# Performance work log

Measured on AMD Instinct MI355X. Metric: run time of the kernel, lower is better.

## Reference

```python
import jax, jax.numpy as jnp
import numpy as np

# ---- module config (init_kwargs) ----
B, CIN, H, W_ = 2, 64, 56, 56
COUT, KH, KW = 128, 3, 3
K = CIN * KH * KW               # 576, reduction dim
ARRAY_ROWS = 128
IN_SLICES = (2, 2, 2, 2)        # 8-bit inputs, 2-bit slices
W_SLICES = (2, 2, 2, 2)         # 8-bit weights, 2-bit slices
N_STEPS_IN = 2 ** sum(IN_SLICES)    # 256, unsigned quantizer
N_STEPS_W = 2 ** sum(W_SLICES)      # 256
ADC_BINS = 256
ADC_STEP = 4.0

def _shifts_masks(slices):
    masks, shifts = [], [0]
    for s in slices[::-1]:
        masks.append((1 << s) - 1)
        shifts.append(s + shifts[-1])
    return np.array(shifts[-2::-1], np.int32), np.array(masks[::-1], np.int32)

_ish, _im = _shifts_masks(IN_SLICES)
_wsh, _wm = _shifts_masks(W_SLICES)
ISH, IM = jnp.asarray(_ish), jnp.asarray(_im)
WSH, WM = jnp.asarray(_wsh), jnp.asarray(_wm)
ISF = jnp.asarray((1 << _ish).astype(np.float32))  # slice recombine weights 2^shift
WSF = jnp.asarray((1 << _wsh).astype(np.float32))


def setup_inputs() -> dict:
    key = jax.random.key(0)
    k1, k2 = jax.random.split(key)
    return {
        "x": jax.random.normal(k1, (B, CIN, H, W_), jnp.float32),
        "w": jax.random.normal(k2, (COUT, CIN, KH, KW), jnp.float32),
    }


def _im2col(x):
    # 3x3 SAME conv patches, ordering [Cin, kh, kw] to match w.reshape(COUT, K)
    xp = jnp.pad(x, ((0, 0), (0, 0), (1, 1), (1, 1)))
    cols = jnp.stack([xp[:, :, i:i + H, j:j + W_]
                      for i in range(KH) for j in range(KW)], axis=2)  # [B,Cin,9,H,W]
    return cols.transpose(0, 3, 4, 1, 2).reshape(B * H * W_, K)  # [Nx, K]


def _quant_unsigned(v, n_steps):
    # Quantizer.offset + Quantizer.forward (unsigned, per-row over dim=-1)
    offs = v.min(axis=-1, keepdims=True)
    vr = v - offs
    step = vr.max(axis=-1, keepdims=True) / (n_steps - 1)
    q = jnp.round(jnp.clip(vr, 0.0, step * n_steps) / step).astype(jnp.int32)
    return q, step[..., 0], offs[..., 0]


def _slice_bits(q, shifts, masks):
    # Slicer.forward: stack (q >> shift) & mask along new leading slice dim
    s = shifts.reshape((-1,) + (1,) * q.ndim)
    m = masks.reshape((-1,) + (1,) * q.ndim)
    return (q[None] >> s) & m


def _chunk(t):
    # Chunker.forward over last dim K
    nb = -(-K // ARRAY_ROWS)
    npb = -(-K // nb)
    pad = nb * npb - K
    t = jnp.pad(t, [(0, 0)] * (t.ndim - 1) + [(0, pad)])
    t = t.reshape(t.shape[:-1] + (nb, npb))
    return jnp.moveaxis(t, -2, 0)  # [nb, ..., npb]


def reference(x, w):
    xf = _im2col(x)                    # [Nx, K]
    wf = w.reshape(COUT, K)            # [Ny, K]
    x_sum = xf.sum(axis=-1)            # [Nx]
    w_sum = wf.sum(axis=-1)            # [Ny]

    xq, x_scale, x_offs = _quant_unsigned(xf, N_STEPS_IN)
    wq, w_scale, w_offs = _quant_unsigned(wf, N_STEPS_W)

    xc = _chunk(_slice_bits(xq, ISH, IM))  # [nb, nis, Nx, npb] int32
    wc = _chunk(_slice_bits(wq, WSH, WM))  # [nb, nws, Ny, npb] int32

    # bit-serial crossbar MACs per (chunk, weight-slice, input-slice)
    z = jnp.einsum('bixk,bwyk->bwixy',
                   xc.astype(jnp.float32), wc.astype(jnp.float32))  # [nb,nws,nis,Nx,Ny]

    # ADC digitization (unsigned, fixed step): quantize then dequantize
    z = jnp.round(jnp.clip(z, 0.0, ADC_STEP * ADC_BINS) / ADC_STEP) * ADC_STEP

    # Chunker.reverse: sum crossbar blocks; Slicer.reverse: shift-weighted sums
    z = z.sum(axis=0)                               # [nws,nis,Nx,Ny]
    z = jnp.einsum('wixy,w,i->xy', z, WSF, ISF)     # [Nx,Ny]

    # dequantize scales and unsigned-offset correction:
    # x.y = sx*sy*(xq.yq) + x_offs*sum(y) + y_offs*sum(x) - x_offs*y_offs*K
    z = z * x_scale[:, None] * w_scale[None, :]
    z = (z + x_offs[:, None] * w_sum[None, :]
           + w_offs[None, :] * x_sum[:, None]
           - x_offs[:, None] * w_offs[None, :] * K)

    return z.reshape(B, H, W_, COUT).transpose(0, 3, 1, 2)  # [B,Cout,H,W]
```

## Files before the change

### kernel.cpp

```cpp
#include <hip/hip_runtime.h>


#define NXROW 6272
#define KDIM  576
#define NPB   116
#define SSTR  656

typedef int i32x4 __attribute__((ext_vector_type(4)));

__device__ __forceinline__ i32x4 slice2b(i32x4 v, int sh) {
    i32x4 r;
    r[0] = (int)(((unsigned)v[0] >> sh) & 0x03030303u);
    r[1] = (int)(((unsigned)v[1] >> sh) & 0x03030303u);
    r[2] = (int)(((unsigned)v[2] >> sh) & 0x03030303u);
    r[3] = (int)(((unsigned)v[3] >> sh) & 0x03030303u);
    return r;
}

__global__ __launch_bounds__(256) void k_q(
    const float* __restrict__ x, const float* __restrict__ w,
    unsigned char* __restrict__ Xq, unsigned char* __restrict__ Wq,
    float* __restrict__ xsc, float* __restrict__ xof, float* __restrict__ xsm,
    float* __restrict__ wsc, float* __restrict__ wof, float* __restrict__ wsm)
{
    __shared__ __align__(16) unsigned char scr[4][SSTR];

    int tid = threadIdx.x, wv = tid >> 6, lane = tid & 63;
    int W = blockIdx.x * 4 + wv;
    unsigned char* myrow = scr[wv];

    if (lane < 16) {
        int col = lane < 12 ? (lane / 3) * 128 + 116 + (lane % 3) * 4
                            : 624 + (lane - 12) * 4;
        *(unsigned int*)(myrow + col) = 0u;
    }

    float v[9];
    unsigned char* dstbase;
    int rl;
    float *sc, *of, *sm;
    int sidx;

    if (W < NXROW) {
        int b = W >= 3136 ? 1 : 0;
        int pos = W - b * 3136;
        int hg = pos / 56, wg = pos - hg * 56;
        const float* xb = x + (size_t)(b * 64) * 3136;
#pragma unroll
        for (int r = 0; r < 9; r++) {
            int k = r * 64 + lane;
            int cin = k / 9;
            int off = k - cin * 9;
            int kh = off / 3;
            int kw = off - kh * 3;
            int hr = hg - 1 + kh, wc = wg - 1 + kw;
            bool ok = ((unsigned)hr < 56u) && ((unsigned)wc < 56u);
            v[r] = ok ? xb[cin * 3136 + hr * 56 + wc] : 0.f;
        }
        dstbase = Xq + (size_t)(W >> 4) * 10240;  rl = W & 15;
        sc = xsc; of = xof; sm = xsm; sidx = W;
    } else {
        int row = W - NXROW;
        const float* wr = w + (size_t)row * KDIM;
#pragma unroll
        for (int r = 0; r < 9; r++) v[r] = wr[r * 64 + lane];
        dstbase = Wq + (size_t)(row >> 4) * 10240;  rl = row & 15;
        sc = wsc; of = wof; sm = wsm; sidx = row;
    }

    float mn = v[0], mx = v[0], s = 0.f;
#pragma unroll
    for (int r = 0; r < 9; r++) { mn = fminf(mn, v[r]); mx = fmaxf(mx, v[r]); s += v[r]; }
#pragma unroll
    for (int off2 = 1; off2 < 64; off2 <<= 1) {
        mn = fminf(mn, __shfl_xor(mn, off2));
        mx = fmaxf(mx, __shfl_xor(mx, off2));
        s += __shfl_xor(s, off2);
    }
    float step = (mx - mn) / 255.0f;
    if (lane == 0) { sc[sidx] = step; of[sidx] = mn; sm[sidx] = s; }

#pragma unroll
    for (int r = 0; r < 9; r++) {
        int q = (int)rintf((v[r] - mn) / step);
        q = q < 0 ? 0 : (q > 255 ? 255 : q);
        int k = r * 64 + lane;
        int ch = k / NPB;
        myrow[k + 12 * ch] = (unsigned char)q;
    }
    __syncthreads();

    if (lane < 40) {
        int u = lane;
        i32x4 seg = *(const i32x4*)(myrow + u * 16);
        int dst16 = (u >> 3) * 128 + ((u >> 2) & 1) * 64 + (u & 3) * 16 + rl;
        *(i32x4*)(dstbase + (size_t)dst16 * 16) = seg;
    }
}

__global__ __launch_bounds__(256) void k_d(
    const unsigned char* __restrict__ Xq, const unsigned char* __restrict__ Wq,
    const float* __restrict__ xscg, const float* __restrict__ xofg,
    const float* __restrict__ xsmg,
    const float* __restrict__ wscg, const float* __restrict__ wofg,
    const float* __restrict__ wsmg, float* __restrict__ out)
{
    __shared__ __align__(16) int pacc[4][64][4];

    int tid = threadIdx.x, wv = tid >> 6, lane = tid & 63;
    int g = lane >> 4, i16 = lane & 15;
    int blk = blockIdx.x;
    int ct = blk & 7, rtile = blk >> 3;
    const unsigned char* xt = Xq + (size_t)rtile * 10240 + lane * 16;
    const unsigned char* wt = Wq + (size_t)ct * 10240 + lane * 16;

    int ish = 6 - 2 * wv;
    const i32x4 zero = {0, 0, 0, 0};
    i32x4 acc4[4] = {{0,0,0,0},{0,0,0,0},{0,0,0,0},{0,0,0,0}};

#pragma unroll
    for (int ch = 0; ch < 5; ch++) {
        i32x4 x0 = *(const i32x4*)(xt + ch * 2048);
        i32x4 x1 = *(const i32x4*)(xt + ch * 2048 + 1024);
        i32x4 w0 = *(const i32x4*)(wt + ch * 2048);
        i32x4 w1 = *(const i32x4*)(wt + ch * 2048 + 1024);
        i32x4 a0 = slice2b(x0, ish), a1 = slice2b(x1, ish);
#pragma unroll
        for (int ws = 0; ws < 4; ws++) {
            i32x4 b0 = slice2b(w0, 6 - 2 * ws);
            i32x4 b1 = slice2b(w1, 6 - 2 * ws);
            i32x4 d = __builtin_amdgcn_mfma_i32_16x16x64_i8(b0, a0, zero, 0, 0, 0);
            d = __builtin_amdgcn_mfma_i32_16x16x64_i8(b1, a1, d, 0, 0, 0);
            int sh = ish + 6 - 2 * ws;
#pragma unroll
            for (int r = 0; r < 4; r++) {
                int z = d[r];
                z = z > 1024 ? 1024 : z;
                int t = (z >> 2) & 1;
                int r4 = (z + 1 + t) & ~3;
                acc4[ws][r] += r4 << sh;
            }
        }
    }

    i32x4 acc;
#pragma unroll
    for (int r = 0; r < 4; r++)
        acc[r] = (acc4[0][r] + acc4[1][r]) + (acc4[2][r] + acc4[3][r]);

    if (wv != 0) *(i32x4*)&pacc[wv][lane][0] = acc;
    __syncthreads();

    if (wv == 0) {
        i32x4 p1 = *(const i32x4*)&pacc[1][lane][0];
        i32x4 p2 = *(const i32x4*)&pacc[2][lane][0];
        i32x4 p3 = *(const i32x4*)&pacc[3][lane][0];
#pragma unroll
        for (int r = 0; r < 4; r++)
            acc[r] = (acc[r] + p1[r]) + (p2[r] + p3[r]);

        int b = rtile >= 196 ? 1 : 0;
        int xrow = rtile * 16 + i16;
        float xs_ = xscg[xrow], xo = xofg[xrow], xsv = xsmg[xrow];
        int hw = (rtile - 196 * b) * 16 + i16;
#pragma unroll
        for (int r = 0; r < 4; r++) {
            int wrow = ct * 16 + g * 4 + r;
            float tt = ((float)acc[r] * xs_) * wscg[wrow];
            float res = ((tt + xo * wsmg[wrow]) + wofg[wrow] * xsv)
                      - (xo * wofg[wrow]) * 576.0f;
            out[(size_t)(b * 128 + wrow) * 3136 + hw] = res;
        }
    }
}

extern "C" void kernel_launch(void* const* d_in, const int* in_sizes, int n_in,
                              void* d_out, int out_size, void* d_ws, size_t ws_size,
                              hipStream_t stream) {
    const float* x = (const float*)d_in[0];
    const float* w = (const float*)d_in[1];
    float* out = (float*)d_out;

    unsigned char* Xq = (unsigned char*)d_ws;
    unsigned char* Wq = Xq + (size_t)392 * 10240;
    float* xsc = (float*)(Wq + 8 * 10240);
    float* xof = xsc + NXROW;
    float* xsm = xof + NXROW;
    float* wsc = xsm + NXROW;
    float* wof = wsc + 128;
    float* wsm = wof + 128;

    hipLaunchKernelGGL(k_q, dim3(1600), dim3(256), 0, stream,
                       x, w, Xq, Wq, xsc, xof, xsm, wsc, wof, wsm);
    hipLaunchKernelGGL(k_d, dim3(3136), dim3(256), 0, stream,
                       Xq, Wq, xsc, xof, xsm, wsc, wof, wsm, out);
}
```

Before: 34.06 us.

## Store quantized X rows linearly and stage tiles through LDS in GEMM kernel

The quantize kernel now writes each X row's padded byte row straight to global memory in row-major form (stride 656). This removes the shared-memory transpose and the __syncthreads on the X path. The MFMA kernel then cooperatively loads a 16-row X tile into LDS and reads its MFMA operands from there. The change trades the strided global scatter for an extra LDS staging step and a barrier in the compute kernel, and it increases the X workspace size and LDS usage.

```diff
diff --git a/kernel.cpp b/kernel.cpp
--- a/kernel.cpp
+++ b/kernel.cpp
@@ -29,23 +29,18 @@
     int W = blockIdx.x * 4 + wv;
     unsigned char* myrow = scr[wv];
 
-    if (lane < 16) {
-        int col = lane < 12 ? (lane / 3) * 128 + 116 + (lane % 3) * 4
-                            : 624 + (lane - 12) * 4;
-        *(unsigned int*)(myrow + col) = 0u;
-    }
-
-    float v[9];
-    unsigned char* dstbase;
-    int rl;
-    float *sc, *of, *sm;
-    int sidx;
-
     if (W < NXROW) {
+        unsigned char* rowp = Xq + (size_t)W * SSTR;
+        if (lane < 16) {
+            int col = lane < 12 ? (lane / 3) * 128 + 116 + (lane % 3) * 4
+                                : 624 + (lane - 12) * 4;
+            *(unsigned int*)(rowp + col) = 0u;
+        }
         int b = W >= 3136 ? 1 : 0;
         int pos = W - b * 3136;
         int hg = pos / 56, wg = pos - hg * 56;
         const float* xb = x + (size_t)(b * 64) * 3136;
+        float v[9];
 #pragma unroll
         for (int r = 0; r < 9; r++) {
             int k = r * 64 + lane;
@@ -57,44 +52,62 @@
             bool ok = ((unsigned)hr < 56u) && ((unsigned)wc < 56u);
             v[r] = ok ? xb[cin * 3136 + hr * 56 + wc] : 0.f;
         }
-        dstbase = Xq + (size_t)(W >> 4) * 10240;  rl = W & 15;
-        sc = xsc; of = xof; sm = xsm; sidx = W;
+        float mn = v[0], mx = v[0], s = 0.f;
+#pragma unroll
+        for (int r = 0; r < 9; r++) { mn = fminf(mn, v[r]); mx = fmaxf(mx, v[r]); s += v[r]; }
+#pragma unroll
+        for (int off2 = 1; off2 < 64; off2 <<= 1) {
+            mn = fminf(mn, __shfl_xor(mn, off2));
+            mx = fmaxf(mx, __shfl_xor(mx, off2));
+            s += __shfl_xor(s, off2);
+        }
+        float step = (mx - mn) / 255.0f;
+        if (lane == 0) { xsc[W] = step; xof[W] = mn; xsm[W] = s; }
+#pragma unroll
+        for (int r = 0; r < 9; r++) {
+            int q = (int)rintf((v[r] - mn) / step);
+            q = q < 0 ? 0 : (q > 255 ? 255 : q);
+            int k = r * 64 + lane;
+            int ch = k / NPB;
+            rowp[k + 12 * ch] = (unsigned char)q;
+        }
     } else {
         int row = W - NXROW;
+        if (lane < 16) {
+            int col = lane < 12 ? (lane / 3) * 128 + 116 + (lane % 3) * 4
+                                : 624 + (lane - 12) * 4;
+            *(unsigned int*)(myrow + col) = 0u;
+        }
         const float* wr = w + (size_t)row * KDIM;
+        float v[9];
 #pragma unroll
         for (int r = 0; r < 9; r++) v[r] = wr[r * 64 + lane];
-        dstbase = Wq + (size_t)(row >> 4) * 10240;  rl = row & 15;
-        sc = wsc; of = wof; sm = wsm; sidx = row;
-    }
-
-    float mn = v[0], mx = v[0], s = 0.f;
-#pragma unroll
-    for (int r = 0; r < 9; r++) { mn = fminf(mn, v[r]); mx = fmaxf(mx, v[r]); s += v[r]; }
-#pragma unroll
-    for (int off2 = 1; off2 < 64; off2 <<= 1) {
-        mn = fminf(mn, __shfl_xor(mn, off2));
-        mx = fmaxf(mx, __shfl_xor(mx, off2));
-        s += __shfl_xor(s, off2);
-    }
-    float step = (mx - mn) / 255.0f;
-    if (lane == 0) { sc[sidx] = step; of[sidx] = mn; sm[sidx] = s; }
-
-#pragma unroll
-    for (int r = 0; r < 9; r++) {
-        int q = (int)rintf((v[r] - mn) / step);
-        q = q < 0 ? 0 : (q > 255 ? 255 : q);
-        int k = r * 64 + lane;
-        int ch = k / NPB;
-        myrow[k + 12 * ch] = (unsigned char)q;
-    }
-    __syncthreads();
-
-    if (lane < 40) {
-        int u = lane;
-        i32x4 seg = *(const i32x4*)(myrow + u * 16);
-        int dst16 = (u >> 3) * 128 + ((u >> 2) & 1) * 64 + (u & 3) * 16 + rl;
-        *(i32x4*)(dstbase + (size_t)dst16 * 16) = seg;
+        float mn = v[0], mx = v[0], s = 0.f;
+#pragma unroll
+        for (int r = 0; r < 9; r++) { mn = fminf(mn, v[r]); mx = fmaxf(mx, v[r]); s += v[r]; }
+#pragma unroll
+        for (int off2 = 1; off2 < 64; off2 <<= 1) {
+            mn = fminf(mn, __shfl_xor(mn, off2));
+            mx = fmaxf(mx, __shfl_xor(mx, off2));
+            s += __shfl_xor(s, off2);
+        }
+        float step = (mx - mn) / 255.0f;
+        if (lane == 0) { wsc[row] = step; wof[row] = mn; wsm[row] = s; }
+#pragma unroll
+        for (int r = 0; r < 9; r++) {
+            int q = (int)rintf((v[r] - mn) / step);
+            q = q < 0 ? 0 : (q > 255 ? 255 : q);
+            int k = r * 64 + lane;
+            int ch = k / NPB;
+            myrow[k + 12 * ch] = (unsigned char)q;
+        }
+        __syncthreads();
+        if (lane < 40) {
+            int u = lane;
+            i32x4 seg = *(const i32x4*)(myrow + u * 16);
+            int dst16 = (u >> 3) * 128 + ((u >> 2) & 1) * 64 + (u & 3) * 16 + (row & 15);
+            *(i32x4*)(Wq + (size_t)(row >> 4) * 10240 + (size_t)dst16 * 16) = seg;
+        }
     }
 }
 
@@ -105,23 +118,29 @@
     const float* __restrict__ wscg, const float* __restrict__ wofg,
     const float* __restrict__ wsmg, float* __restrict__ out)
 {
+    __shared__ __align__(16) unsigned char xlds[16 * SSTR];
     __shared__ __align__(16) int pacc[4][64][4];
 
     int tid = threadIdx.x, wv = tid >> 6, lane = tid & 63;
     int g = lane >> 4, i16 = lane & 15;
     int blk = blockIdx.x;
     int ct = blk & 7, rtile = blk >> 3;
-    const unsigned char* xt = Xq + (size_t)rtile * 10240 + lane * 16;
+    const unsigned char* xt = Xq + (size_t)rtile * (16 * SSTR);
     const unsigned char* wt = Wq + (size_t)ct * 10240 + lane * 16;
 
+    for (int idx = tid; idx < 16 * SSTR / 16; idx += 256)
+        *(i32x4*)(xlds + (size_t)idx * 16) = *(const i32x4*)(xt + (size_t)idx * 16);
+    __syncthreads();
+
+    const unsigned char* xp = xlds + i16 * SSTR + g * 16;
     int ish = 6 - 2 * wv;
     const i32x4 zero = {0, 0, 0, 0};
     i32x4 acc4[4] = {{0,0,0,0},{0,0,0,0},{0,0,0,0},{0,0,0,0}};
 
 #pragma unroll
     for (int ch = 0; ch < 5; ch++) {
-        i32x4 x0 = *(const i32x4*)(xt + ch * 2048);
-        i32x4 x1 = *(const i32x4*)(xt + ch * 2048 + 1024);
+        i32x4 x0 = *(const i32x4*)(xp + ch * 128);
+        i32x4 x1 = *(const i32x4*)(xp + ch * 128 + 64);
         i32x4 w0 = *(const i32x4*)(wt + ch * 2048);
         i32x4 w1 = *(const i32x4*)(wt + ch * 2048 + 1024);
         i32x4 a0 = slice2b(x0, ish), a1 = slice2b(x1, ish);
@@ -182,7 +201,7 @@
     float* out = (float*)d_out;
 
     unsigned char* Xq = (unsigned char*)d_ws;
-    unsigned char* Wq = Xq + (size_t)392 * 10240;
+    unsigned char* Wq = Xq + (size_t)NXROW * SSTR;
     float* xsc = (float*)(Wq + 8 * 10240);
     float* xof = xsc + NXROW;
     float* xsm = xof + NXROW;
```

Result: slower. 35.46 us (+4.1%).
